# Kernel optimization log

Hardware: AMD Instinct MI355X
Metric: run time of the kernel (lower is better)

## Reference

```python
import jax, jax.numpy as jnp
import numpy as np

VAR0, VAR1 = 0.1, 0.2
POS_TH, NEG_TH = 0.5, 0.5
NEG_POS_RATIO = 10

def point_form(c):
    # center-size (cx,cy,w,h) -> corners (x1,y1,x2,y2)
    return jnp.concatenate([c[..., :2] - c[..., 2:] / 2, c[..., :2] + c[..., 2:] / 2], axis=-1)

def iou(a, b):
    # corner-form boxes, broadcastable [..., 4]
    lt = jnp.maximum(a[..., :2], b[..., :2])
    rb = jnp.minimum(a[..., 2:], b[..., 2:])
    wh = jnp.clip(rb - lt, 0.0)
    inter = wh[..., 0] * wh[..., 1]
    area_a = (a[..., 2] - a[..., 0]) * (a[..., 3] - a[..., 1])
    area_b = (b[..., 2] - b[..., 0]) * (b[..., 3] - b[..., 1])
    return inter / (area_a + area_b - inter)

def encode(matched, priors):
    # matched: corner-form gt boxes; priors: center-size anchors
    g_cxcy = ((matched[..., :2] + matched[..., 2:]) * 0.5 - priors[..., :2]) / (VAR0 * priors[..., 2:])
    g_wh = jnp.log((matched[..., 2:] - matched[..., :2]) / priors[..., 2:]) / VAR1
    return jnp.concatenate([g_cxcy, g_wh], axis=-1)

def smooth_l1(d):
    ad = jnp.abs(d)
    return jnp.where(ad < 1.0, 0.5 * ad * ad, ad - 0.5)

def setup_inputs() -> dict:
    key = jax.random.key(0)
    ks = jax.random.split(key, 8)
    B, O, A = 8, 32, 16384
    cxy = jax.random.uniform(ks[0], (A, 2), minval=0.1, maxval=0.9)
    wh = jax.random.uniform(ks[1], (A, 2), minval=0.05, maxval=0.3)
    anchors = jnp.concatenate([cxy, wh], axis=-1)  # [A,4] center-size
    # ground-truth boxes jittered around random anchors so matching finds positives
    idx = jax.random.randint(ks[2], (B, O), 0, A)
    base = point_form(anchors)[idx]  # [B,O,4] corner form
    boxes = base + jax.random.uniform(ks[3], (B, O, 4), minval=-0.01, maxval=0.01)
    counts = jax.random.randint(ks[4], (B,), 4, O)  # valid objects per image
    pad = jnp.arange(O)[None, :] >= counts[:, None]
    cls = jax.random.randint(ks[5], (B, O), 0, 2)
    true_classes = jnp.where(pad, -1, cls).astype(jnp.int32)
    true_boxes = jnp.where(pad[..., None], -1.0, boxes)
    pred_boxes = 0.5 * jax.random.normal(ks[6], (B, A, 4))
    pred_classes = jax.random.normal(ks[7], (B, A, 2))
    return dict(pred_boxes=pred_boxes, pred_classes=pred_classes,
                true_boxes=true_boxes, true_classes=true_classes, anchors=anchors)

def detection_loss(pred_boxes, pred_classes, true_boxes, true_classes, anchors):
    dtype = pred_boxes.dtype
    pad = true_classes < 0  # [B,O]
    # --- anchor matching (IoU between corner-form anchors and gt boxes) ---
    overlap = iou(point_form(anchors)[None, None, :, :], true_boxes[:, :, None, :])  # [B,O,A]
    overlap = jnp.where(pad[..., None], -1.0, overlap)
    best = overlap.max(axis=1, keepdims=True)  # best gt per anchor
    positive = (jnp.abs(best - overlap) < 1e-6) & (overlap > POS_TH)  # [B,O,A]
    negative = overlap.max(axis=1) < NEG_TH  # [B,A]
    n_pos = positive.sum()
    denom = jnp.maximum(n_pos, 1).astype(dtype)
    # --- box loss: SmoothL1(sum) on encoded positives only ---
    dummy = jnp.array([0.3, 0.3, 0.5, 0.5], dtype)  # valid dummy box for padded slots (masked out)
    tb = jnp.where(pad[..., None], dummy, true_boxes)
    enc = encode(tb[:, :, None, :], anchors[None, None, :, :])  # [B,O,A,4]
    d = jnp.where(positive[..., None], pred_boxes[:, None, :, :] - enc, 0.0)
    box_loss = 1.0 * smooth_l1(d).sum() / denom
    # --- class loss: positives + hard-negative mining, weighted CE mean ---
    logp = jax.nn.log_softmax(pred_classes, axis=-1)  # [B,A,2]
    cls = jnp.clip(true_classes, 0, 1)
    ce_pos = -jnp.where((cls == 1)[:, :, None], logp[:, None, :, 1], logp[:, None, :, 0])  # [B,O,A]
    w = jnp.where(cls == 1, 4.0, 1.0)[:, :, None]
    sum_pos = jnp.sum(positive * w * ce_pos)
    wsum_pos = jnp.sum(positive * w)
    # negatives: target class 0 (weight 1); mining rank == CE value
    neg_ce = jnp.where(negative, -logp[..., 0], -jnp.inf).reshape(-1)  # [B*A]
    sorted_desc = jnp.sort(neg_ce)[::-1]
    n_neg = negative.sum()
    k = jnp.minimum(NEG_POS_RATIO * n_pos, n_neg)
    take = jnp.arange(sorted_desc.shape[0]) < k
    sum_neg = jnp.sum(jnp.where(take, sorted_desc, 0.0))
    cls_loss = 10.0 * (sum_pos + sum_neg) / jnp.maximum(wsum_pos + k.astype(dtype), 1e-6) / denom
    total = box_loss + cls_loss
    return box_loss, cls_loss, total

def reference(pred_boxes, pred_classes, true_boxes, true_classes, anchors):
    return detection_loss(pred_boxes, pred_classes, true_boxes, true_classes, anchors)
```

## Files before the change

kernel.cpp:

```cpp
#include <hip/hip_runtime.h>
#include <math.h>

#define NOBJ  32
#define NANCH 16384
#define NTOT  131072
#define NBLK  16
#define MARK  0xFFFFFFFFu

#define OFF_SLOTS 64
#define OFF_H1C   4160
#define OFF_H2C   20544
#define OFF_H3C   36928
#define OFF_FLAG  37952
#define OFF_FSL   38208
#define OFF_ZERO_BEG  OFF_H1C
#define OFF_ZERO_WORDS 34064
#define OFF_BITS  38224

__device__ __forceinline__ float smooth_l1f(float d) {
    float ad = fabsf(d);
    return ad < 1.0f ? 0.5f * ad * ad : ad - 0.5f;
}

__global__ __launch_bounds__(256) void dl_main(
    const float* __restrict__ pred_boxes,
    const float* __restrict__ pred_classes,
    const float* __restrict__ true_boxes,
    const int*   __restrict__ true_classes,
    const float* __restrict__ anchors,
    unsigned int* __restrict__ ws)
{
    __shared__ float s_tb[NOBJ * 4];
    __shared__ int   s_tc[NOBJ];
    __shared__ int   s_ri[4][2];
    __shared__ float s_rf[4][3];

    if (blockIdx.x < 135) {
        int zw = blockIdx.x * 256 + threadIdx.x;
        if (zw < OFF_ZERO_WORDS) ws[OFF_ZERO_BEG + zw] = 0u;
    }

    int idx = blockIdx.x * 256 + threadIdx.x;
    int b = idx >> 14;
    int a = idx & (NANCH - 1);
    if (threadIdx.x < NOBJ * 4) s_tb[threadIdx.x] = true_boxes[b * NOBJ * 4 + threadIdx.x];
    if (threadIdx.x < NOBJ)     s_tc[threadIdx.x] = true_classes[b * NOBJ + threadIdx.x];
    __syncthreads();

    float4 anc = reinterpret_cast<const float4*>(anchors)[a];
    float ax1 = anc.x - anc.z * 0.5f;
    float ay1 = anc.y - anc.w * 0.5f;
    float ax2 = anc.x + anc.z * 0.5f;
    float ay2 = anc.y + anc.w * 0.5f;
    float area_a = (ax2 - ax1) * (ay2 - ay1);

    float ov[NOBJ];
    float best = -3.402823466e38f;
#pragma unroll
    for (int o = 0; o < NOBJ; ++o) {
        float v;
        if (s_tc[o] < 0) {
            v = -1.0f;
        } else {
            float bx1 = s_tb[o * 4 + 0], by1 = s_tb[o * 4 + 1];
            float bx2 = s_tb[o * 4 + 2], by2 = s_tb[o * 4 + 3];
            float ltx = fmaxf(ax1, bx1), lty = fmaxf(ay1, by1);
            float rbx = fminf(ax2, bx2), rby = fminf(ay2, by2);
            float w = fmaxf(rbx - ltx, 0.0f), h = fmaxf(rby - lty, 0.0f);
            float inter = w * h;
            float area_b = (bx2 - bx1) * (by2 - by1);
            v = inter / (area_a + area_b - inter);
        }
        ov[o] = v;
        best = fmaxf(best, v);
    }

    float2 pc = reinterpret_cast<const float2*>(pred_classes)[idx];
    float mx = fmaxf(pc.x, pc.y);
    float lse = mx + logf(expf(pc.x - mx) + expf(pc.y - mx));
    float l0 = pc.x - lse;
    float l1 = pc.y - lse;

    unsigned bits = MARK;
    int isneg = 0;
    if (best < 0.5f) { bits = __float_as_uint(-l0); isneg = 1; }
    ws[OFF_BITS + idx] = bits;

    float4 pb = reinterpret_cast<const float4*>(pred_boxes)[idx];
    int npos = 0; float boxs = 0.f, poss = 0.f, wsum = 0.f;
#pragma unroll
    for (int o = 0; o < NOBJ; ++o) {
        float v = ov[o];
        if (fabsf(best - v) < 1e-6f && v > 0.5f) {
            ++npos;
            float bx1 = s_tb[o * 4 + 0], by1 = s_tb[o * 4 + 1];
            float bx2 = s_tb[o * 4 + 2], by2 = s_tb[o * 4 + 3];
            float gcx = ((bx1 + bx2) * 0.5f - anc.x) / (0.1f * anc.z);
            float gcy = ((by1 + by2) * 0.5f - anc.y) / (0.1f * anc.w);
            float gw  = logf((bx2 - bx1) / anc.z) / 0.2f;
            float gh  = logf((by2 - by1) / anc.w) / 0.2f;
            boxs += smooth_l1f(pb.x - gcx) + smooth_l1f(pb.y - gcy)
                  + smooth_l1f(pb.z - gw)  + smooth_l1f(pb.w - gh);
            int c = s_tc[o];
            float w = (c == 1) ? 4.0f : 1.0f;
            poss += w * ((c == 1) ? -l1 : -l0);
            wsum += w;
        }
    }

    int ip = npos, ng = isneg;
    float fb = boxs, fp = poss, fw = wsum;
#pragma unroll
    for (int off = 32; off; off >>= 1) {
        ip += __shfl_down(ip, off);
        ng += __shfl_down(ng, off);
        fb += __shfl_down(fb, off);
        fp += __shfl_down(fp, off);
        fw += __shfl_down(fw, off);
    }
    int wid = threadIdx.x >> 6, lane = threadIdx.x & 63;
    if (lane == 0) {
        s_ri[wid][0] = ip; s_ri[wid][1] = ng;
        s_rf[wid][0] = fb; s_rf[wid][1] = fp; s_rf[wid][2] = fw;
    }
    __syncthreads();
    if (threadIdx.x == 0) {
        int tp = 0, tn = 0; float t2 = 0.f, t3 = 0.f, t4 = 0.f;
        for (int wv = 0; wv < 4; ++wv) {
            tp += s_ri[wv][0]; tn += s_ri[wv][1];
            t2 += s_rf[wv][0]; t3 += s_rf[wv][1]; t4 += s_rf[wv][2];
        }
        int base = OFF_SLOTS + blockIdx.x * 8;
        ((int*)ws)[base + 0] = tp;
        ((int*)ws)[base + 1] = tn;
        ((float*)ws)[base + 2] = t2;
        ((float*)ws)[base + 3] = t3;
        ((float*)ws)[base + 4] = t4;
    }
}


__device__ __forceinline__ void gbar(unsigned* ws, unsigned phase) {
    __syncthreads();
    if (threadIdx.x < 64) {
        if (threadIdx.x == 0) {
            __threadfence();
            __hip_atomic_store(ws + OFF_FLAG + blockIdx.x * 16, phase,
                               __ATOMIC_RELEASE, __HIP_MEMORY_SCOPE_AGENT);
        }
        bool ok;
        do {
            unsigned v = (threadIdx.x < NBLK)
                ? __hip_atomic_load(ws + OFF_FLAG + threadIdx.x * 16,
                                    __ATOMIC_ACQUIRE, __HIP_MEMORY_SCOPE_AGENT)
                : phase;
            ok = __all(v >= phase);
            if (!ok) __builtin_amdgcn_s_sleep(1);
        } while (!ok);
    }
    __syncthreads();
}

__global__ __launch_bounds__(1024) void dl_select(unsigned int* __restrict__ ws,
                                                  float* __restrict__ out)
{
    __shared__ unsigned hrep[4][4096];
    __shared__ int      wtot[16];
    __shared__ int      s_wi[16][2];
    __shared__ float    s_wf[16][3];
    __shared__ int      sh[4];

    const int t = threadIdx.x, wave = t >> 6, lane = t & 63, rep = wave >> 2;
    const bool b0 = (blockIdx.x == 0);
    unsigned* hflat = &hrep[0][0];

    uint4 va = reinterpret_cast<const uint4*>(ws + OFF_BITS + blockIdx.x * 8192)[t * 2];
    uint4 vc = reinterpret_cast<const uint4*>(ws + OFF_BITS + blockIdx.x * 8192)[t * 2 + 1];
    unsigned vb[8] = { va.x, va.y, va.z, va.w, vc.x, vc.y, vc.z, vc.w };

    for (int i = t; i < 16384; i += 1024) hflat[i] = 0u;

    int np = 0, nn = 0; float fb = 0.f, fp = 0.f, fw = 0.f;
    if (t < 512) {
        const unsigned* sl = ws + OFF_SLOTS + t * 8;
        np = (int)sl[0]; nn = (int)sl[1];
        fb = __uint_as_float(sl[2]); fp = __uint_as_float(sl[3]); fw = __uint_as_float(sl[4]);
    }
#pragma unroll
    for (int o = 32; o; o >>= 1) {
        np += __shfl_down(np, o); nn += __shfl_down(nn, o);
        fb += __shfl_down(fb, o); fp += __shfl_down(fp, o); fw += __shfl_down(fw, o);
    }
    if (lane == 0) {
        s_wi[wave][0] = np; s_wi[wave][1] = nn;
        s_wf[wave][0] = fb; s_wf[wave][1] = fp; s_wf[wave][2] = fw;
    }
    __syncthreads();
    np = 0; nn = 0; fb = fp = fw = 0.f;
    for (int w = 0; w < 16; ++w) {
        np += s_wi[w][0]; nn += s_wi[w][1];
        fb += s_wf[w][0]; fp += s_wf[w][1]; fw += s_wf[w][2];
    }

    long long k10 = 10LL * (long long)np;
    int k = (int)((k10 < (long long)nn) ? k10 : (long long)nn);
    float denom = (float)(np > 1 ? np : 1);
    float box_loss = fb / denom;

    if (k == 0) {
        if (b0 && t == 0) {
            float cls = 10.0f * fp / fmaxf(fw, 1e-6f) / denom;
            out[0] = box_loss; out[1] = cls; out[2] = box_loss + cls;
        }
        return;
    }

#pragma unroll
    for (int j = 0; j < 8; ++j) {
        unsigned b = vb[j];
        if (b != MARK) atomicAdd(&hrep[rep][b >> 20], 1u);
    }
    __syncthreads();
    {
        unsigned* g = ws + OFF_H1C + (blockIdx.x & 3) * 4096;
#pragma unroll
        for (int i = 0; i < 4; ++i) {
            int bkt = t * 4 + i;
            unsigned c = hrep[0][bkt] + hrep[1][bkt] + hrep[2][bkt] + hrep[3][bkt];
            if (c) atomicAdd(g + bkt, c);
        }
    }
    unsigned phase = 1;
    gbar(ws, phase);

    auto sel12 = [&](int off, int target) {
        unsigned c4[4] = {0u, 0u, 0u, 0u};
#pragma unroll
        for (int r = 0; r < 4; ++r) {
            uint4 u = reinterpret_cast<const uint4*>(ws + off + r * 4096)[t];
            c4[0] += u.x; c4[1] += u.y; c4[2] += u.z; c4[3] += u.w;
        }
        int cc = (int)(c4[0] + c4[1] + c4[2] + c4[3]);
        int v = cc;
#pragma unroll
        for (int o = 1; o < 64; o <<= 1) {
            int u2 = __shfl_down(v, o);
            if (lane + o < 64) v += u2;
        }
        if (lane == 0) wtot[wave] = v;
        __syncthreads();
        int S = v;
        for (int w = wave + 1; w < 16; ++w) S += wtot[w];
        if (S >= target && S - cc < target) {
            int cum = S - cc;
            for (int b = 3; b >= 0; --b) {
                int cb = (int)c4[b];
                if (cum + cb >= target) { sh[0] = t * 4 + b; sh[1] = target - cum; sh[2] = cb; break; }
                cum += cb;
            }
        }
        __syncthreads();
    };

    sel12(OFF_H1C, k);
    int b1 = sh[0], r1 = sh[1];
    unsigned THR = 0; int ge = 0, rrem = 0, resolved = 0;
    if (sh[1] == sh[2]) { THR = (unsigned)b1 << 20; ge = 1; resolved = 1; }

    if (!resolved) {
        for (int i = t; i < 16384; i += 1024) hflat[i] = 0u;
        __syncthreads();
#pragma unroll
        for (int j = 0; j < 8; ++j) {
            unsigned b = vb[j];
            if ((int)(b >> 20) == b1) atomicAdd(&hrep[rep][(b >> 8) & 0xFFFu], 1u);
        }
        __syncthreads();
        {
            unsigned* g = ws + OFF_H2C + (blockIdx.x & 3) * 4096;
#pragma unroll
            for (int i = 0; i < 4; ++i) {
                int bkt = t * 4 + i;
                unsigned c = hrep[0][bkt] + hrep[1][bkt] + hrep[2][bkt] + hrep[3][bkt];
                if (c) atomicAdd(g + bkt, c);
            }
        }
        gbar(ws, ++phase);
        sel12(OFF_H2C, r1);
        int b2 = sh[0], r2 = sh[1];
        unsigned pfx = ((unsigned)b1 << 12) | (unsigned)b2;
        if (sh[1] == sh[2]) { THR = pfx << 8; ge = 1; resolved = 1; }

        if (!resolved) {
            for (int i = t; i < 16384; i += 1024) hflat[i] = 0u;
            __syncthreads();
#pragma unroll
            for (int j = 0; j < 8; ++j) {
                unsigned b = vb[j];
                if ((b >> 8) == pfx) atomicAdd(&hrep[rep][b & 0xFFu], 1u);
            }
            __syncthreads();
            if (t < 256) {
                unsigned c = hrep[0][t] + hrep[1][t] + hrep[2][t] + hrep[3][t];
                if (c) atomicAdd(ws + OFF_H3C + (blockIdx.x & 3) * 256 + t, c);
            }
            gbar(ws, ++phase);
            int c = 0;
            if (t < 256)
                for (int r = 0; r < 4; ++r) c += (int)ws[OFF_H3C + r * 256 + t];
            int v = c;
#pragma unroll
            for (int o = 1; o < 64; o <<= 1) {
                int u2 = __shfl_down(v, o);
                if (lane + o < 64) v += u2;
            }
            if (lane == 0) wtot[wave] = v;
            __syncthreads();
            int S = v;
            for (int w = wave + 1; w < 16; ++w) S += wtot[w];
            if (S >= r2 && S - c < r2) { sh[0] = t; sh[1] = r2 - (S - c); }
            __syncthreads();
            THR = (pfx << 8) | (unsigned)sh[0];
            rrem = sh[1];
            ge = 0;
        }
    }

    float loc = 0.f;
#pragma unroll
    for (int j = 0; j < 8; ++j) {
        unsigned b = vb[j];
        if (b != MARK && (ge ? (b >= THR) : (b > THR))) loc += __uint_as_float(b);
    }
#pragma unroll
    for (int o = 32; o; o >>= 1) loc += __shfl_down(loc, o);
    if (lane == 0) s_wf[wave][0] = loc;
    __syncthreads();
    if (t == 0) {
        float s = 0.f;
        for (int w = 0; w < 16; ++w) s += s_wf[w][0];
        ((float*)ws)[OFF_FSL + blockIdx.x] = s;
    }
    gbar(ws, ++phase);
    if (b0 && t < 64) {
        float s = (t < NBLK) ? ((const float*)ws)[OFF_FSL + t] : 0.f;
#pragma unroll
        for (int o = 32; o; o >>= 1) s += __shfl_down(s, o);
        if (t == 0) {
            float sneg = s + (ge ? 0.f : (float)rrem * __uint_as_float(THR));
            float cls = 10.0f * (fp + sneg) / fmaxf(fw + (float)k, 1e-6f) / denom;
            out[0] = box_loss; out[1] = cls; out[2] = box_loss + cls;
        }
    }
}

extern "C" void kernel_launch(void* const* d_in, const int* in_sizes, int n_in,
                              void* d_out, int out_size, void* d_ws, size_t ws_size,
                              hipStream_t stream)
{
    const float* pred_boxes   = (const float*)d_in[0];
    const float* pred_classes = (const float*)d_in[1];
    const float* true_boxes   = (const float*)d_in[2];
    const int*   true_classes = (const int*)d_in[3];
    const float* anchors      = (const float*)d_in[4];
    unsigned int* ws = (unsigned int*)d_ws;

    dl_main<<<NTOT / 256, 256, 0, stream>>>(pred_boxes, pred_classes, true_boxes,
                                            true_classes, anchors, ws);
    dl_select<<<NBLK, 1024, 0, stream>>>(ws, (float*)d_out);
}
```

Before: 31.27 us.

## Fuse matching and radix-select into one persistent kernel with grid barriers

Merges the per-anchor matching kernel and the hard-negative radix-select kernel into a single 128-block, 1024-thread kernel. Each thread keeps its negative-CE bits in a register instead of writing them to global memory and reading them back. The first-level histogram is built in the same pass as the IoU matching. The early-exit shortcuts are removed so all three select levels always run, and the final threshold sum is computed from the level-3 histogram in block 0. Workspace zeroing moves to a separate small kernel. In exchange, the kernel now needs 128 co-resident blocks for its spin-wait grid barriers, and each barrier polls 128 flags.

```diff
diff --git a/kernel.cpp b/kernel.cpp
--- a/kernel.cpp
+++ b/kernel.cpp
@@ -4,47 +4,78 @@
 #define NOBJ  32
 #define NANCH 16384
 #define NTOT  131072
-#define NBLK  16
+#define NBLK  128
+#define NREP  8
 #define MARK  0xFFFFFFFFu
 
 #define OFF_SLOTS 64
-#define OFF_H1C   4160
-#define OFF_H2C   20544
-#define OFF_H3C   36928
-#define OFF_FLAG  37952
-#define OFF_FSL   38208
+#define OFF_H1C   1088
+#define OFF_H2C   33856
+#define OFF_H3C   66624
+#define OFF_FLAG  68672
+#define OFF_FSL   70720
 #define OFF_ZERO_BEG  OFF_H1C
-#define OFF_ZERO_WORDS 34064
-#define OFF_BITS  38224
+#define OFF_ZERO_WORDS 69632
 
 __device__ __forceinline__ float smooth_l1f(float d) {
     float ad = fabsf(d);
     return ad < 1.0f ? 0.5f * ad * ad : ad - 0.5f;
 }
 
-__global__ __launch_bounds__(256) void dl_main(
+__global__ __launch_bounds__(256) void dl_zero(unsigned int* __restrict__ ws)
+{
+    int i = blockIdx.x * 256 + threadIdx.x;
+    for (int w = i; w < OFF_ZERO_WORDS; w += 128 * 256) ws[OFF_ZERO_BEG + w] = 0u;
+}
+
+__device__ __forceinline__ void gbar(unsigned* ws, unsigned phase) {
+    __syncthreads();
+    if (threadIdx.x < 64) {
+        if (threadIdx.x == 0) {
+            __threadfence();
+            __hip_atomic_store(ws + OFF_FLAG + blockIdx.x * 16, phase,
+                               __ATOMIC_RELEASE, __HIP_MEMORY_SCOPE_AGENT);
+        }
+        bool ok;
+        do {
+            unsigned v0 = __hip_atomic_load(ws + OFF_FLAG + threadIdx.x * 16,
+                                            __ATOMIC_ACQUIRE, __HIP_MEMORY_SCOPE_AGENT);
+            unsigned v1 = __hip_atomic_load(ws + OFF_FLAG + (64 + threadIdx.x) * 16,
+                                            __ATOMIC_ACQUIRE, __HIP_MEMORY_SCOPE_AGENT);
+            ok = __all(v0 >= phase && v1 >= phase);
+            if (!ok) __builtin_amdgcn_s_sleep(1);
+        } while (!ok);
+    }
+    __syncthreads();
+}
+
+__global__ __launch_bounds__(1024) void dl_fused(
     const float* __restrict__ pred_boxes,
     const float* __restrict__ pred_classes,
     const float* __restrict__ true_boxes,
     const int*   __restrict__ true_classes,
     const float* __restrict__ anchors,
-    unsigned int* __restrict__ ws)
+    unsigned int* __restrict__ ws,
+    float* __restrict__ out)
 {
+    __shared__ unsigned hrep[4][4096];
     __shared__ float s_tb[NOBJ * 4];
     __shared__ int   s_tc[NOBJ];
-    __shared__ int   s_ri[4][2];
-    __shared__ float s_rf[4][3];
-
-    if (blockIdx.x < 135) {
-        int zw = blockIdx.x * 256 + threadIdx.x;
-        if (zw < OFF_ZERO_WORDS) ws[OFF_ZERO_BEG + zw] = 0u;
-    }
-
-    int idx = blockIdx.x * 256 + threadIdx.x;
-    int b = idx >> 14;
-    int a = idx & (NANCH - 1);
-    if (threadIdx.x < NOBJ * 4) s_tb[threadIdx.x] = true_boxes[b * NOBJ * 4 + threadIdx.x];
-    if (threadIdx.x < NOBJ)     s_tc[threadIdx.x] = true_classes[b * NOBJ + threadIdx.x];
+    __shared__ int   wtot[16];
+    __shared__ int   s_wi[16][2];
+    __shared__ float s_wf[16][3];
+    __shared__ int   sh[4];
+
+    const int t = threadIdx.x, wave = t >> 6, lane = t & 63, rep = wave >> 2;
+    const bool b0 = (blockIdx.x == 0);
+    unsigned* hflat = &hrep[0][0];
+
+    const int idx = blockIdx.x * 1024 + t;
+    const int b = idx >> 14;
+    const int a = idx & (NANCH - 1);
+    if (t < NOBJ * 4) s_tb[t] = true_boxes[b * NOBJ * 4 + t];
+    if (t < NOBJ)     s_tc[t] = true_classes[b * NOBJ + t];
+    for (int i = t; i < 16384; i += 1024) hflat[i] = 0u;
     __syncthreads();
 
     float4 anc = reinterpret_cast<const float4*>(anchors)[a];
@@ -84,7 +115,6 @@
     unsigned bits = MARK;
     int isneg = 0;
     if (best < 0.5f) { bits = __float_as_uint(-l0); isneg = 1; }
-    ws[OFF_BITS + idx] = bits;
 
     float4 pb = reinterpret_cast<const float4*>(pred_boxes)[idx];
     int npos = 0; float boxs = 0.f, poss = 0.f, wsum = 0.f;
@@ -108,104 +138,64 @@
         }
     }
 
+    if (bits != MARK) atomicAdd(&hrep[rep][bits >> 20], 1u);
+
     int ip = npos, ng = isneg;
-    float fb = boxs, fp = poss, fw = wsum;
-#pragma unroll
-    for (int off = 32; off; off >>= 1) {
-        ip += __shfl_down(ip, off);
-        ng += __shfl_down(ng, off);
-        fb += __shfl_down(fb, off);
-        fp += __shfl_down(fp, off);
-        fw += __shfl_down(fw, off);
-    }
-    int wid = threadIdx.x >> 6, lane = threadIdx.x & 63;
+    float fb = boxs, fp2 = poss, fw2 = wsum;
+#pragma unroll
+    for (int o = 32; o; o >>= 1) {
+        ip += __shfl_down(ip, o); ng += __shfl_down(ng, o);
+        fb += __shfl_down(fb, o); fp2 += __shfl_down(fp2, o); fw2 += __shfl_down(fw2, o);
+    }
     if (lane == 0) {
-        s_ri[wid][0] = ip; s_ri[wid][1] = ng;
-        s_rf[wid][0] = fb; s_rf[wid][1] = fp; s_rf[wid][2] = fw;
-    }
-    __syncthreads();
-    if (threadIdx.x == 0) {
+        s_wi[wave][0] = ip; s_wi[wave][1] = ng;
+        s_wf[wave][0] = fb; s_wf[wave][1] = fp2; s_wf[wave][2] = fw2;
+    }
+    __syncthreads();
+    {
+        unsigned* g = ws + OFF_H1C + (blockIdx.x & (NREP - 1)) * 4096;
+#pragma unroll
+        for (int i = 0; i < 4; ++i) {
+            int bkt = t * 4 + i;
+            unsigned c = hrep[0][bkt] + hrep[1][bkt] + hrep[2][bkt] + hrep[3][bkt];
+            if (c) atomicAdd(g + bkt, c);
+        }
+    }
+    if (t == 0) {
         int tp = 0, tn = 0; float t2 = 0.f, t3 = 0.f, t4 = 0.f;
-        for (int wv = 0; wv < 4; ++wv) {
-            tp += s_ri[wv][0]; tn += s_ri[wv][1];
-            t2 += s_rf[wv][0]; t3 += s_rf[wv][1]; t4 += s_rf[wv][2];
-        }
-        int base = OFF_SLOTS + blockIdx.x * 8;
-        ((int*)ws)[base + 0] = tp;
-        ((int*)ws)[base + 1] = tn;
-        ((float*)ws)[base + 2] = t2;
-        ((float*)ws)[base + 3] = t3;
-        ((float*)ws)[base + 4] = t4;
-    }
-}
-
-
-__device__ __forceinline__ void gbar(unsigned* ws, unsigned phase) {
-    __syncthreads();
-    if (threadIdx.x < 64) {
-        if (threadIdx.x == 0) {
-            __threadfence();
-            __hip_atomic_store(ws + OFF_FLAG + blockIdx.x * 16, phase,
-                               __ATOMIC_RELEASE, __HIP_MEMORY_SCOPE_AGENT);
-        }
-        bool ok;
-        do {
-            unsigned v = (threadIdx.x < NBLK)
-                ? __hip_atomic_load(ws + OFF_FLAG + threadIdx.x * 16,
-                                    __ATOMIC_ACQUIRE, __HIP_MEMORY_SCOPE_AGENT)
-                : phase;
-            ok = __all(v >= phase);
-            if (!ok) __builtin_amdgcn_s_sleep(1);
-        } while (!ok);
-    }
-    __syncthreads();
-}
-
-__global__ __launch_bounds__(1024) void dl_select(unsigned int* __restrict__ ws,
-                                                  float* __restrict__ out)
-{
-    __shared__ unsigned hrep[4][4096];
-    __shared__ int      wtot[16];
-    __shared__ int      s_wi[16][2];
-    __shared__ float    s_wf[16][3];
-    __shared__ int      sh[4];
-
-    const int t = threadIdx.x, wave = t >> 6, lane = t & 63, rep = wave >> 2;
-    const bool b0 = (blockIdx.x == 0);
-    unsigned* hflat = &hrep[0][0];
-
-    uint4 va = reinterpret_cast<const uint4*>(ws + OFF_BITS + blockIdx.x * 8192)[t * 2];
-    uint4 vc = reinterpret_cast<const uint4*>(ws + OFF_BITS + blockIdx.x * 8192)[t * 2 + 1];
-    unsigned vb[8] = { va.x, va.y, va.z, va.w, vc.x, vc.y, vc.z, vc.w };
-
-    for (int i = t; i < 16384; i += 1024) hflat[i] = 0u;
-
-    int np = 0, nn = 0; float fb = 0.f, fp = 0.f, fw = 0.f;
-    if (t < 512) {
+        for (int w = 0; w < 16; ++w) {
+            tp += s_wi[w][0]; tn += s_wi[w][1];
+            t2 += s_wf[w][0]; t3 += s_wf[w][1]; t4 += s_wf[w][2];
+        }
+        unsigned* sl = ws + OFF_SLOTS + blockIdx.x * 8;
+        sl[0] = (unsigned)tp; sl[1] = (unsigned)tn;
+        sl[2] = __float_as_uint(t2); sl[3] = __float_as_uint(t3); sl[4] = __float_as_uint(t4);
+    }
+    gbar(ws, 1u);
+
+    int np = 0, nn = 0; float fbx = 0.f, fp = 0.f, fw = 0.f;
+    if (t < NBLK) {
         const unsigned* sl = ws + OFF_SLOTS + t * 8;
         np = (int)sl[0]; nn = (int)sl[1];
-        fb = __uint_as_float(sl[2]); fp = __uint_as_float(sl[3]); fw = __uint_as_float(sl[4]);
+        fbx = __uint_as_float(sl[2]); fp = __uint_as_float(sl[3]); fw = __uint_as_float(sl[4]);
     }
 #pragma unroll
     for (int o = 32; o; o >>= 1) {
         np += __shfl_down(np, o); nn += __shfl_down(nn, o);
-        fb += __shfl_down(fb, o); fp += __shfl_down(fp, o); fw += __shfl_down(fw, o);
-    }
-    if (lane == 0) {
+        fbx += __shfl_down(fbx, o); fp += __shfl_down(fp, o); fw += __shfl_down(fw, o);
+    }
+    if (lane == 0 && wave < 2) {
         s_wi[wave][0] = np; s_wi[wave][1] = nn;
-        s_wf[wave][0] = fb; s_wf[wave][1] = fp; s_wf[wave][2] = fw;
-    }
-    __syncthreads();
-    np = 0; nn = 0; fb = fp = fw = 0.f;
-    for (int w = 0; w < 16; ++w) {
-        np += s_wi[w][0]; nn += s_wi[w][1];
-        fb += s_wf[w][0]; fp += s_wf[w][1]; fw += s_wf[w][2];
-    }
+        s_wf[wave][0] = fbx; s_wf[wave][1] = fp; s_wf[wave][2] = fw;
+    }
+    __syncthreads();
+    np = s_wi[0][0] + s_wi[1][0]; nn = s_wi[0][1] + s_wi[1][1];
+    fbx = s_wf[0][0] + s_wf[1][0]; fp = s_wf[0][1] + s_wf[1][1]; fw = s_wf[0][2] + s_wf[1][2];
 
     long long k10 = 10LL * (long long)np;
     int k = (int)((k10 < (long long)nn) ? k10 : (long long)nn);
     float denom = (float)(np > 1 ? np : 1);
-    float box_loss = fb / denom;
+    float box_loss = fbx / denom;
 
     if (k == 0) {
         if (b0 && t == 0) {
@@ -215,28 +205,10 @@
         return;
     }
 
-#pragma unroll
-    for (int j = 0; j < 8; ++j) {
-        unsigned b = vb[j];
-        if (b != MARK) atomicAdd(&hrep[rep][b >> 20], 1u);
-    }
-    __syncthreads();
-    {
-        unsigned* g = ws + OFF_H1C + (blockIdx.x & 3) * 4096;
-#pragma unroll
-        for (int i = 0; i < 4; ++i) {
-            int bkt = t * 4 + i;
-            unsigned c = hrep[0][bkt] + hrep[1][bkt] + hrep[2][bkt] + hrep[3][bkt];
-            if (c) atomicAdd(g + bkt, c);
-        }
-    }
-    unsigned phase = 1;
-    gbar(ws, phase);
-
     auto sel12 = [&](int off, int target) {
         unsigned c4[4] = {0u, 0u, 0u, 0u};
 #pragma unroll
-        for (int r = 0; r < 4; ++r) {
+        for (int r = 0; r < NREP; ++r) {
             uint4 u = reinterpret_cast<const uint4*>(ws + off + r * 4096)[t];
             c4[0] += u.x; c4[1] += u.y; c4[2] += u.z; c4[3] += u.w;
         }
@@ -253,9 +225,9 @@
         for (int w = wave + 1; w < 16; ++w) S += wtot[w];
         if (S >= target && S - cc < target) {
             int cum = S - cc;
-            for (int b = 3; b >= 0; --b) {
-                int cb = (int)c4[b];
-                if (cum + cb >= target) { sh[0] = t * 4 + b; sh[1] = target - cum; sh[2] = cb; break; }
+            for (int bq = 3; bq >= 0; --bq) {
+                int cb = (int)c4[bq];
+                if (cum + cb >= target) { sh[0] = t * 4 + bq; sh[1] = target - cum; break; }
                 cum += cb;
             }
         }
@@ -264,93 +236,79 @@
 
     sel12(OFF_H1C, k);
     int b1 = sh[0], r1 = sh[1];
-    unsigned THR = 0; int ge = 0, rrem = 0, resolved = 0;
-    if (sh[1] == sh[2]) { THR = (unsigned)b1 << 20; ge = 1; resolved = 1; }
-
-    if (!resolved) {
-        for (int i = t; i < 16384; i += 1024) hflat[i] = 0u;
-        __syncthreads();
-#pragma unroll
-        for (int j = 0; j < 8; ++j) {
-            unsigned b = vb[j];
-            if ((int)(b >> 20) == b1) atomicAdd(&hrep[rep][(b >> 8) & 0xFFFu], 1u);
-        }
-        __syncthreads();
-        {
-            unsigned* g = ws + OFF_H2C + (blockIdx.x & 3) * 4096;
-#pragma unroll
-            for (int i = 0; i < 4; ++i) {
-                int bkt = t * 4 + i;
-                unsigned c = hrep[0][bkt] + hrep[1][bkt] + hrep[2][bkt] + hrep[3][bkt];
-                if (c) atomicAdd(g + bkt, c);
-            }
-        }
-        gbar(ws, ++phase);
-        sel12(OFF_H2C, r1);
-        int b2 = sh[0], r2 = sh[1];
-        unsigned pfx = ((unsigned)b1 << 12) | (unsigned)b2;
-        if (sh[1] == sh[2]) { THR = pfx << 8; ge = 1; resolved = 1; }
-
-        if (!resolved) {
-            for (int i = t; i < 16384; i += 1024) hflat[i] = 0u;
-            __syncthreads();
-#pragma unroll
-            for (int j = 0; j < 8; ++j) {
-                unsigned b = vb[j];
-                if ((b >> 8) == pfx) atomicAdd(&hrep[rep][b & 0xFFu], 1u);
-            }
-            __syncthreads();
-            if (t < 256) {
-                unsigned c = hrep[0][t] + hrep[1][t] + hrep[2][t] + hrep[3][t];
-                if (c) atomicAdd(ws + OFF_H3C + (blockIdx.x & 3) * 256 + t, c);
-            }
-            gbar(ws, ++phase);
-            int c = 0;
-            if (t < 256)
-                for (int r = 0; r < 4; ++r) c += (int)ws[OFF_H3C + r * 256 + t];
-            int v = c;
-#pragma unroll
-            for (int o = 1; o < 64; o <<= 1) {
-                int u2 = __shfl_down(v, o);
-                if (lane + o < 64) v += u2;
-            }
-            if (lane == 0) wtot[wave] = v;
-            __syncthreads();
-            int S = v;
-            for (int w = wave + 1; w < 16; ++w) S += wtot[w];
-            if (S >= r2 && S - c < r2) { sh[0] = t; sh[1] = r2 - (S - c); }
-            __syncthreads();
-            THR = (pfx << 8) | (unsigned)sh[0];
-            rrem = sh[1];
-            ge = 0;
-        }
-    }
-
-    float loc = 0.f;
-#pragma unroll
-    for (int j = 0; j < 8; ++j) {
-        unsigned b = vb[j];
-        if (b != MARK && (ge ? (b >= THR) : (b > THR))) loc += __uint_as_float(b);
-    }
+
+    for (int i = t; i < 16384; i += 1024) hflat[i] = 0u;
+    __syncthreads();
+    if ((int)(bits >> 20) == b1) atomicAdd(&hrep[rep][(bits >> 8) & 0xFFFu], 1u);
+    __syncthreads();
+    {
+        unsigned* g = ws + OFF_H2C + (blockIdx.x & (NREP - 1)) * 4096;
+#pragma unroll
+        for (int i = 0; i < 4; ++i) {
+            int bkt = t * 4 + i;
+            unsigned c = hrep[0][bkt] + hrep[1][bkt] + hrep[2][bkt] + hrep[3][bkt];
+            if (c) atomicAdd(g + bkt, c);
+        }
+    }
+    gbar(ws, 2u);
+
+    sel12(OFF_H2C, r1);
+    int b2 = sh[0], r2 = sh[1];
+    unsigned pfx = ((unsigned)b1 << 12) | (unsigned)b2;
+
+    if (t < 1024) hrep[t >> 8][t & 255] = 0u;
+    __syncthreads();
+    if ((bits >> 8) == pfx) atomicAdd(&hrep[rep][bits & 0xFFu], 1u);
+    float loc = (bits != MARK && (bits >> 8) > pfx) ? __uint_as_float(bits) : 0.f;
 #pragma unroll
     for (int o = 32; o; o >>= 1) loc += __shfl_down(loc, o);
     if (lane == 0) s_wf[wave][0] = loc;
     __syncthreads();
+    if (t < 256) {
+        unsigned c = hrep[0][t] + hrep[1][t] + hrep[2][t] + hrep[3][t];
+        if (c) atomicAdd(ws + OFF_H3C + (blockIdx.x & (NREP - 1)) * 256 + t, c);
+    }
     if (t == 0) {
         float s = 0.f;
         for (int w = 0; w < 16; ++w) s += s_wf[w][0];
         ((float*)ws)[OFF_FSL + blockIdx.x] = s;
     }
-    gbar(ws, ++phase);
-    if (b0 && t < 64) {
-        float s = (t < NBLK) ? ((const float*)ws)[OFF_FSL + t] : 0.f;
-#pragma unroll
-        for (int o = 32; o; o >>= 1) s += __shfl_down(s, o);
-        if (t == 0) {
-            float sneg = s + (ge ? 0.f : (float)rrem * __uint_as_float(THR));
-            float cls = 10.0f * (fp + sneg) / fmaxf(fw + (float)k, 1e-6f) / denom;
-            out[0] = box_loss; out[1] = cls; out[2] = box_loss + cls;
-        }
+    gbar(ws, 3u);
+
+    if (!b0) return;
+    int c = 0;
+    if (t < 256)
+        for (int r = 0; r < NREP; ++r) c += (int)ws[OFF_H3C + r * 256 + t];
+    int v = c;
+#pragma unroll
+    for (int o = 1; o < 64; o <<= 1) {
+        int u2 = __shfl_down(v, o);
+        if (lane + o < 64) v += u2;
+    }
+    if (lane == 0) wtot[wave] = v;
+    __syncthreads();
+    int S = v;
+    for (int w = wave + 1; w < 16; ++w) S += wtot[w];
+    if (t < 256 && S >= r2 && S - c < r2) { sh[0] = t; sh[1] = r2 - (S - c); }
+    __syncthreads();
+    int cut = sh[0], rrem = sh[1];
+
+    float term = 0.f;
+    if (t < 256) {
+        float vv = __uint_as_float((pfx << 8) | (unsigned)t);
+        if (t > cut) term = (float)c * vv;
+        else if (t == cut) term = (float)rrem * vv;
+    }
+    if (t < NBLK) term += ((const float*)ws)[OFF_FSL + t];
+#pragma unroll
+    for (int o = 32; o; o >>= 1) term += __shfl_down(term, o);
+    if (lane == 0) s_wf[wave][0] = term;
+    __syncthreads();
+    if (t == 0) {
+        float sneg = 0.f;
+        for (int w = 0; w < 16; ++w) sneg += s_wf[w][0];
+        float cls = 10.0f * (fp + sneg) / fmaxf(fw + (float)k, 1e-6f) / denom;
+        out[0] = box_loss; out[1] = cls; out[2] = box_loss + cls;
     }
 }
 
@@ -365,7 +323,7 @@
     const float* anchors      = (const float*)d_in[4];
     unsigned int* ws = (unsigned int*)d_ws;
 
-    dl_main<<<NTOT / 256, 256, 0, stream>>>(pred_boxes, pred_classes, true_boxes,
-                                            true_classes, anchors, ws);
-    dl_select<<<NBLK, 1024, 0, stream>>>(ws, (float*)d_out);
-}
+    dl_zero<<<128, 256, 0, stream>>>(ws);
+    dl_fused<<<NBLK, 1024, 0, stream>>>(pred_boxes, pred_classes, true_boxes,
+                                        true_classes, anchors, ws, (float*)d_out);
+}
```

New measurement: 55.07 us. +76.1%, slower.
